# Performance work log

Measured on AMD Instinct MI355X. Metric: run time of the kernel, lower is better.

Reference implementation:

```python
import jax, jax.numpy as jnp
import numpy as np

DIM = 256; HEADS = 8; WS = 7; ALPHA = 0.5
HD = DIM // HEADS                      # head_dim = 32
GH = int(HEADS * ALPHA); LH = HEADS - GH   # 4 global / 4 local heads
GD = GH * HD; LD = LH * HD             # 128 / 128
HID = int(DIM * 4.0)                   # mlp hidden = 1024
SCALE = HD ** -0.5


def ln(x, g, b, eps=1e-5):
    m = jnp.mean(x, -1, keepdims=True)
    v = jnp.var(x, -1, keepdims=True)
    return (x - m) * jax.lax.rsqrt(v + eps) * g + b


def setup_inputs() -> dict:
    key = jax.random.key(0)
    ks = jax.random.split(key, 12)
    B, H, W = 4, 112, 112
    N = H * W
    def p(k, shape, s=0.02):
        return jax.random.normal(k, shape, jnp.float32) * s
    return {
        'x': jax.random.normal(ks[0], (B, N, DIM), jnp.float32),
        'x_reverse': jax.random.normal(ks[1], (B, N, DIM), jnp.float32),
        'g1': jnp.ones((DIM,), jnp.float32), 'b1': jnp.zeros((DIM,), jnp.float32),
        'g2': jnp.ones((DIM,), jnp.float32), 'b2': jnp.zeros((DIM,), jnp.float32),
        'Gq_w': p(ks[2], (DIM, GD)), 'Gq_b': jnp.zeros((GD,), jnp.float32),
        'Gkv_w': p(ks[3], (DIM, 2 * GD)), 'Gkv_b': jnp.zeros((2 * GD,), jnp.float32),
        'Gp_w': p(ks[4], (GD, GD)), 'Gp_b': jnp.zeros((GD,), jnp.float32),
        'Lq_w': p(ks[5], (DIM, LD)), 'Lq_b': jnp.zeros((LD,), jnp.float32),
        'Lkv_w': p(ks[6], (DIM, 2 * LD)), 'Lkv_b': jnp.zeros((2 * LD,), jnp.float32),
        'Lp_w': p(ks[7], (LD, LD)), 'Lp_b': jnp.zeros((LD,), jnp.float32),
        'fc1_w': p(ks[8], (DIM, HID)), 'fc1_b': jnp.zeros((HID,), jnp.float32),
        'dw_w': p(ks[9], (HID, 1, 3, 3), 0.05), 'dw_b': jnp.zeros((HID,), jnp.float32),
        'fc2_w': p(ks[10], (HID, DIM)), 'fc2_b': jnp.zeros((DIM,), jnp.float32),
        'H': 112, 'W': 112,
    }


def reference(x, x_reverse, g1, b1, g2, b2,
              Gq_w, Gq_b, Gkv_w, Gkv_b, Gp_w, Gp_b,
              Lq_w, Lq_b, Lkv_w, Lkv_b, Lp_w, Lp_b,
              fc1_w, fc1_b, dw_w, dw_b, fc2_w, fc2_b, H, W):
    B, N, C = x.shape
    assert H % WS == 0 and W % WS == 0  # shapes chosen so no padding branch
    xn = ln(x, g1, b1).reshape(B, H, W, C)
    xrn = ln(x_reverse, g1, b1).reshape(B, H, W, C)

    # ---- Global attention: queries from every pixel, kv from avg-pooled (ws x ws) grid
    q = (xn.reshape(B, N, C) @ Gq_w + Gq_b).reshape(B, N, GH, HD)
    pooled = xrn.reshape(B, H // WS, WS, W // WS, WS, C).mean(axis=(2, 4)).reshape(B, -1, C)
    kv = (pooled @ Gkv_w + Gkv_b).reshape(B, -1, 2, GH, HD)
    k, v = kv[:, :, 0], kv[:, :, 1]
    a = jax.nn.softmax(jnp.einsum('bnhd,bmhd->bhnm', q, k) * SCALE, axis=-1)
    g_out = jnp.einsum('bhnm,bmhd->bnhd', a, v).reshape(B, H, W, GD) @ Gp_w + Gp_b

    # ---- Local windowed attention (ws x ws non-overlapping windows)
    hg, wg = H // WS, W // WS
    TG, T = hg * wg, WS * WS
    def windows(t):
        return t.reshape(B, hg, WS, wg, WS, C).transpose(0, 1, 3, 2, 4, 5).reshape(B, TG, T, C)
    xw, xrw = windows(xn), windows(xrn)
    ql = (xw @ Lq_w + Lq_b).reshape(B, TG, T, LH, HD)
    kvl = (xrw @ Lkv_w + Lkv_b).reshape(B, TG, T, 2, LH, HD)
    kl, vl = kvl[:, :, :, 0], kvl[:, :, :, 1]
    al = jax.nn.softmax(jnp.einsum('bgqhd,bgkhd->bghqk', ql, kl) * SCALE, axis=-1)
    lo = jnp.einsum('bghqk,bgkhd->bgqhd', al, vl).reshape(B, hg, wg, WS, WS, LD)
    lo = lo.transpose(0, 1, 3, 2, 4, 5).reshape(B, H, W, LD) @ Lp_w + Lp_b

    x = x + jnp.concatenate([g_out, lo], axis=-1).reshape(B, N, C)

    # ---- DWMlp: fc1 -> depthwise 3x3 conv -> GELU -> fc2
    h = ln(x, g2, b2) @ fc1_w + fc1_b
    himg = h.reshape(B, H, W, HID).transpose(0, 3, 1, 2)
    himg = jax.lax.conv_general_dilated(
        himg, dw_w, (1, 1), 'SAME', feature_group_count=HID,
        dimension_numbers=('NCHW', 'OIHW', 'NCHW')) + dw_b[None, :, None, None]
    h = jax.nn.gelu(himg.reshape(B, HID, N).transpose(0, 2, 1), approximate=False)
    return x + (h @ fc2_w + fc2_b)
```

## Files before the change

### kernel.cpp

```cpp
#include <hip/hip_runtime.h>
#include <hip/hip_bf16.h>
#include <math.h>

typedef __hip_bfloat16 bf16;
typedef __attribute__((ext_vector_type(8))) short bf16x8;
typedef __attribute__((ext_vector_type(4))) float f32x4;

static constexpr int B_  = 4;
static constexpr int Hh  = 112, Ww = 112;
static constexpr int Nn  = Hh * Ww;
static constexpr int Cc  = 256;
static constexpr int M_  = B_ * Nn;
static constexpr int GH_ = 4;
static constexpr int GD_ = 128;
static constexpr int LD_ = 128;
static constexpr int HID_ = 1024;
static constexpr int TG_ = 256;
static constexpr int T__ = 49;
static constexpr float SCALE_ = 0.17677669529663687f;

__device__ __forceinline__ float toF(const bf16 v)  { return __bfloat162float(v); }
__device__ __forceinline__ float toF(const float v) { return v; }
__device__ __forceinline__ void st_out(float* p, float v) { *p = v; }
__device__ __forceinline__ void st_out(bf16* p, float v)  { *p = __float2bfloat16(v); }

__device__ __forceinline__ void gload_lds16(const bf16* g, bf16* l) {
  using gvoid = const __attribute__((address_space(1))) void;
  using lvoid = __attribute__((address_space(3))) void;
  __builtin_amdgcn_global_load_lds((gvoid*)g, (lvoid*)l, 16, 0, 0);
}

__device__ __forceinline__ int win_row_map(int r) {
  int b  = r / Nn;
  int rr = r - b * Nn;
  int g  = rr / T__;
  int t  = rr - g * T__;
  int gh = g >> 4, gw = g & 15;
  int i  = t / 7,  j  = t - i * 7;
  int n  = (gh * 7 + i) * Ww + gw * 7 + j;
  return b * Nn + n;
}

__global__ void guard_fill_kernel(float* out) {
  out[threadIdx.x + blockIdx.x * 256] = 1.0e6f;
}

__global__ __launch_bounds__(256) void convert_all_kernel(
    const float* __restrict__ s0, const float* __restrict__ s1,
    const float* __restrict__ s2, const float* __restrict__ s3,
    const float* __restrict__ s4, const float* __restrict__ s5,
    const float* __restrict__ s6, const float* __restrict__ s7,
    bf16* __restrict__ wt) {
  int idx = blockIdx.x * 256 + threadIdx.x;
  const float* W; int K, N, base;
  if      (idx < 32768)  { W = s0; K = 256;  N = 128;  base = 0; }
  else if (idx < 98304)  { W = s1; K = 256;  N = 256;  base = 32768; }
  else if (idx < 114688) { W = s2; K = 128;  N = 128;  base = 98304; }
  else if (idx < 147456) { W = s3; K = 256;  N = 128;  base = 114688; }
  else if (idx < 212992) { W = s4; K = 256;  N = 256;  base = 147456; }
  else if (idx < 229376) { W = s5; K = 128;  N = 128;  base = 212992; }
  else if (idx < 491520) { W = s6; K = 256;  N = 1024; base = 229376; }
  else                   { W = s7; K = 1024; N = 256;  base = 491520; }
  int loc = idx - base;
  int n = loc / K, k = loc - n * K;
  wt[idx] = __float2bfloat16(W[(size_t)k * N + n]);
}

__global__ __launch_bounds__(256) void ln_dual_kernel(const float* __restrict__ x,
                                                      const float* __restrict__ xr,
                                                      const float* __restrict__ g,
                                                      const float* __restrict__ bta,
                                                      bf16* __restrict__ xn,
                                                      bf16* __restrict__ xrn) {
  const int tid = threadIdx.x;
  const int row = blockIdx.x * 4 + (tid >> 6);
  const int lane = tid & 63;
  const int c0 = lane * 4;
  const float* src = blockIdx.y ? xr : x;
  bf16* dst = blockIdx.y ? xrn : xn;
  float4 v = *(const float4*)(src + (size_t)row * Cc + c0);
  float s  = v.x + v.y + v.z + v.w;
  float ss = v.x * v.x + v.y * v.y + v.z * v.z + v.w * v.w;
  #pragma unroll
  for (int off = 1; off < 64; off <<= 1) {
    s  += __shfl_xor(s, off);
    ss += __shfl_xor(ss, off);
  }
  float mean = s * (1.0f / Cc);
  float var  = ss * (1.0f / Cc) - mean * mean;
  float r = rsqrtf(var + 1e-5f);
  float4 gv = *(const float4*)(g + c0);
  float4 bv = *(const float4*)(bta + c0);
  bf16 o[4];
  o[0] = __float2bfloat16((v.x - mean) * r * gv.x + bv.x);
  o[1] = __float2bfloat16((v.y - mean) * r * gv.y + bv.y);
  o[2] = __float2bfloat16((v.z - mean) * r * gv.z + bv.z);
  o[3] = __float2bfloat16((v.w - mean) * r * gv.w + bv.w);
  *(uint2*)(dst + (size_t)row * Cc + c0) = *(uint2*)o;
}

__global__ __launch_bounds__(64) void pool_kernel(const bf16* __restrict__ xrn,
                                                  bf16* __restrict__ pooled) {
  const int lane = threadIdx.x;
  const int c0 = lane * 4;
  const int g  = blockIdx.x;
  const int b  = blockIdx.y;
  const int gh = g >> 4, gw = g & 15;
  float acc[4] = {};
  union U4 { uint2 u; bf16 e[4]; };
  #pragma unroll
  for (int i = 0; i < 7; i++)
    for (int j = 0; j < 7; j++) {
      int n = (gh * 7 + i) * Ww + gw * 7 + j;
      U4 r4;
      r4.u = *(const uint2*)(xrn + ((size_t)b * Nn + n) * Cc + c0);
      #pragma unroll
      for (int u = 0; u < 4; u++) acc[u] += toF(r4.e[u]);
    }
  bf16 o[4];
  #pragma unroll
  for (int u = 0; u < 4; u++) o[u] = __float2bfloat16(acc[u] * (1.0f / 49.0f));
  *(uint2*)(pooled + ((size_t)b * TG_ + g) * Cc + c0) = *(uint2*)o;
}

template <typename OutT, bool WIN_A, bool RES>
__global__ __launch_bounds__(256) void mfma_gemm_kernel(const bf16* __restrict__ A,
                                                        const bf16* __restrict__ Wt,
                                                        const float* __restrict__ bias,
                                                        const float* __restrict__ res,
                                                        OutT* __restrict__ out,
                                                        int M, int N, int K) {
  __shared__ __align__(16) bf16 As[128 * 32];
  __shared__ __align__(16) bf16 Bs[128 * 32];
  const int tid = threadIdx.x;
  const int bm = blockIdx.y * 128, bn = blockIdx.x * 128;
  const int lane = tid & 63, w = tid >> 6;
  const int wm = (w >> 1) * 64, wn = (w & 1) * 64;

  const int srow0 = w * 32 + (lane >> 2);
  const int srow1 = srow0 + 16;
  const int kq    = (lane & 3) * 8;
  const int ar0 = bm + srow0, ar1 = bm + srow1;
  const int as0 = WIN_A ? win_row_map(ar0) : ar0;
  const int as1 = WIN_A ? win_row_map(ar1) : ar1;
  const bf16* Ag0 = A  + (size_t)as0 * K + kq;
  const bf16* Ag1 = A  + (size_t)as1 * K + kq;
  const bf16* Bg0 = Wt + (size_t)(bn + srow0) * K + kq;
  const bf16* Bg1 = Wt + (size_t)(bn + srow1) * K + kq;
  bf16* Al0 = &As[srow0 * 32 + kq];
  bf16* Al1 = &As[srow1 * 32 + kq];
  bf16* Bl0 = &Bs[srow0 * 32 + kq];
  bf16* Bl1 = &Bs[srow1 * 32 + kq];

  f32x4 acc[4][4];
  #pragma unroll
  for (int i = 0; i < 4; i++)
    #pragma unroll
    for (int j = 0; j < 4; j++) acc[i][j] = (f32x4){0.f, 0.f, 0.f, 0.f};

  const int r16  = lane & 15;
  const int koct = (lane >> 4) * 8;
  const int mrow = wm + r16;
  const int nrow = wn + r16;

  for (int k0 = 0; k0 < K; k0 += 32) {
    gload_lds16(Ag0 + k0, Al0);
    gload_lds16(Ag1 + k0, Al1);
    gload_lds16(Bg0 + k0, Bl0);
    gload_lds16(Bg1 + k0, Bl1);
    __syncthreads();
    bf16x8 af[4], bfr[4];
    #pragma unroll
    for (int i = 0; i < 4; i++) af[i]  = *(const bf16x8*)&As[(mrow + i * 16) * 32 + koct];
    #pragma unroll
    for (int j = 0; j < 4; j++) bfr[j] = *(const bf16x8*)&Bs[(nrow + j * 16) * 32 + koct];
    #pragma unroll
    for (int i = 0; i < 4; i++)
      #pragma unroll
      for (int j = 0; j < 4; j++)
        acc[i][j] = __builtin_amdgcn_mfma_f32_16x16x32_bf16(af[i], bfr[j], acc[i][j], 0, 0, 0);
    __syncthreads();
  }

  const int r0 = (lane >> 4) * 4;
  #pragma unroll
  for (int j = 0; j < 4; j++) {
    const int col = bn + wn + j * 16 + r16;
    const float bv = bias[col];
    #pragma unroll
    for (int i = 0; i < 4; i++) {
      const int rowb = bm + wm + i * 16 + r0;
      #pragma unroll
      for (int r = 0; r < 4; r++) {
        size_t ro = (size_t)(rowb + r) * N + col;
        float v = acc[i][j][r] + bv;
        if (RES) v += res[ro];
        st_out(out + ro, v);
      }
    }
  }
}

__global__ __launch_bounds__(256) void gattn_kernel(const bf16* __restrict__ q,
                                                    const bf16* __restrict__ kv,
                                                    bf16* __restrict__ out) {
  __shared__ __align__(16) bf16 Ks[256][40];
  __shared__ __align__(16) bf16 Vt[32][264];
  __shared__ __align__(16) bf16 Ps[4][32][40];
  const int tid = threadIdx.x;
  const int lane = tid & 63, w = tid >> 6;
  const int h = blockIdx.y, b = blockIdx.z;
  const int n0 = blockIdx.x * 128;
  const int r16 = lane & 15, oct = (lane >> 4) * 8;
  const bf16* kvb = kv + (size_t)b * TG_ * 256;

  {
    const int key = tid;
    const bf16* kp = kvb + (size_t)key * 256 + h * 32;
    *(uint4*)&Ks[key][0]  = *(const uint4*)(kp);
    *(uint4*)&Ks[key][8]  = *(const uint4*)(kp + 8);
    *(uint4*)&Ks[key][16] = *(const uint4*)(kp + 16);
    *(uint4*)&Ks[key][24] = *(const uint4*)(kp + 24);
    union { uint4 u[4]; bf16 e[32]; } vv;
    vv.u[0] = *(const uint4*)(kp + 128);
    vv.u[1] = *(const uint4*)(kp + 136);
    vv.u[2] = *(const uint4*)(kp + 144);
    vv.u[3] = *(const uint4*)(kp + 152);
    #pragma unroll
    for (int d = 0; d < 32; d++) Vt[d][key] = vv.e[d];
  }
  const size_t qbase0 = ((size_t)(b * Nn + n0 + w * 32 + r16)) * GD_ + h * 32 + oct;
  bf16x8 aq0 = *(const bf16x8*)(q + qbase0);
  bf16x8 aq1 = *(const bf16x8*)(q + qbase0 + (size_t)16 * GD_);
  __syncthreads();

  f32x4 rs0 = {0.f, 0.f, 0.f, 0.f}, rs1 = {0.f, 0.f, 0.f, 0.f};
  f32x4 ov[2][2];
  #pragma unroll
  for (int i = 0; i < 2; i++)
    #pragma unroll
    for (int dt = 0; dt < 2; dt++) ov[i][dt] = (f32x4){0.f, 0.f, 0.f, 0.f};

  for (int c0 = 0; c0 < 256; c0 += 32) {
    #pragma unroll
    for (int t = 0; t < 2; t++) {
      bf16x8 bk = *(const bf16x8*)&Ks[c0 + t * 16 + r16][oct];
      f32x4 s0 = __builtin_amdgcn_mfma_f32_16x16x32_bf16(aq0, bk, (f32x4){0.f,0.f,0.f,0.f}, 0, 0, 0);
      f32x4 s1 = __builtin_amdgcn_mfma_f32_16x16x32_bf16(aq1, bk, (f32x4){0.f,0.f,0.f,0.f}, 0, 0, 0);
      const int prow = (lane >> 4) * 4;
      const int pcol = t * 16 + r16;
      #pragma unroll
      for (int r = 0; r < 4; r++) {
        bf16 pb0 = __float2bfloat16(__expf(s0[r] * SCALE_));
        bf16 pb1 = __float2bfloat16(__expf(s1[r] * SCALE_));
        rs0[r] += toF(pb0);
        rs1[r] += toF(pb1);
        Ps[w][prow + r][pcol]      = pb0;
        Ps[w][16 + prow + r][pcol] = pb1;
      }
    }
    bf16x8 ap0 = *(const bf16x8*)&Ps[w][r16][oct];
    bf16x8 ap1 = *(const bf16x8*)&Ps[w][16 + r16][oct];
    #pragma unroll
    for (int dt = 0; dt < 2; dt++) {
      bf16x8 bv = *(const bf16x8*)&Vt[dt * 16 + r16][c0 + oct];
      ov[0][dt] = __builtin_amdgcn_mfma_f32_16x16x32_bf16(ap0, bv, ov[0][dt], 0, 0, 0);
      ov[1][dt] = __builtin_amdgcn_mfma_f32_16x16x32_bf16(ap1, bv, ov[1][dt], 0, 0, 0);
    }
  }
  #pragma unroll
  for (int off = 1; off < 16; off <<= 1) {
    #pragma unroll
    for (int r = 0; r < 4; r++) {
      rs0[r] += __shfl_xor(rs0[r], off);
      rs1[r] += __shfl_xor(rs1[r], off);
    }
  }
  const int orow0 = b * Nn + n0 + w * 32 + (lane >> 4) * 4;
  #pragma unroll
  for (int r = 0; r < 4; r++) {
    float inv0 = 1.0f / rs0[r];
    float inv1 = 1.0f / rs1[r];
    size_t ro0 = (size_t)(orow0 + r) * GD_ + h * 32;
    size_t ro1 = ro0 + (size_t)16 * GD_;
    #pragma unroll
    for (int dt = 0; dt < 2; dt++) {
      out[ro0 + dt * 16 + r16] = __float2bfloat16(ov[0][dt][r] * inv0);
      out[ro1 + dt * 16 + r16] = __float2bfloat16(ov[1][dt][r] * inv1);
    }
  }
}

__global__ __launch_bounds__(256) void lattn_kernel(const bf16* __restrict__ ql,
                                                    const bf16* __restrict__ kvl,
                                                    bf16* __restrict__ out) {
  __shared__ __align__(16) bf16 Ks[4][64][40];
  __shared__ __align__(16) bf16 Vt[4][32][72];
  __shared__ __align__(16) bf16 Ps[4][64][72];
  const int tid = threadIdx.x;
  const int lane = tid & 63, w = tid >> 6;
  const int g = blockIdx.x, b = blockIdx.y;
  const int r16 = lane & 15, oct = (lane >> 4) * 8;
  const size_t wbase = ((size_t)b * TG_ + g) * T__;

  for (int u = tid; u < T__ * 32; u += 256) {
    int m = u >> 5, c8 = u & 31;
    union { uint4 q4; bf16 e[8]; } ch;
    ch.q4 = *(const uint4*)(kvl + (wbase + m) * 256 + c8 * 8);
    if (c8 < 16) {
      int h = c8 >> 2, d0 = (c8 & 3) * 8;
      *(uint4*)&Ks[h][m][d0] = ch.q4;
    } else {
      int cv = c8 - 16;
      int h = cv >> 2, d0 = (cv & 3) * 8;
      #pragma unroll
      for (int e = 0; e < 8; e++) Vt[h][d0 + e][m] = ch.e[e];
    }
  }
  for (int z = tid; z < 4 * 32 * 15; z += 256) {
    int h = z / 480, rem = z - h * 480;
    int d = rem / 15, key = 49 + (rem - d * 15);
    Vt[h][d][key] = __float2bfloat16(0.f);
  }
  bf16x8 aq[4];
  #pragma unroll
  for (int i = 0; i < 4; i++) {
    int qr = 16 * i + r16;
    if (qr > 48) qr = 48;
    aq[i] = *(const bf16x8*)(ql + (wbase + qr) * LD_ + w * 32 + oct);
  }
  __syncthreads();

  f32x4 s[4][4];
  #pragma unroll
  for (int j = 0; j < 4; j++) {
    bf16x8 bk = *(const bf16x8*)&Ks[w][16 * j + r16][oct];
    #pragma unroll
    for (int i = 0; i < 4; i++)
      s[i][j] = __builtin_amdgcn_mfma_f32_16x16x32_bf16(aq[i], bk, (f32x4){0.f,0.f,0.f,0.f}, 0, 0, 0);
  }

  const int prow = (lane >> 4) * 4;
  float rs[4][4];
  #pragma unroll
  for (int i = 0; i < 4; i++) {
    #pragma unroll
    for (int r = 0; r < 4; r++) {
      float acc = 0.f;
      #pragma unroll
      for (int j = 0; j < 4; j++) {
        float p = __expf(s[i][j][r] * SCALE_);
        if (j == 3 && r16 != 0) p = 0.f;
        bf16 pb = __float2bfloat16(p);
        Ps[w][16 * i + prow + r][16 * j + r16] = pb;
        acc += toF(pb);
      }
      #pragma unroll
      for (int off = 1; off < 16; off <<= 1) acc += __shfl_xor(acc, off);
      rs[i][r] = acc;
    }
  }

  f32x4 ov[4][2];
  #pragma unroll
  for (int i = 0; i < 4; i++) {
    ov[i][0] = (f32x4){0.f, 0.f, 0.f, 0.f};
    ov[i][1] = (f32x4){0.f, 0.f, 0.f, 0.f};
  }
  #pragma unroll
  for (int kc = 0; kc < 2; kc++) {
    bf16x8 bv0 = *(const bf16x8*)&Vt[w][r16][kc * 32 + oct];
    bf16x8 bv1 = *(const bf16x8*)&Vt[w][16 + r16][kc * 32 + oct];
    #pragma unroll
    for (int i = 0; i < 4; i++) {
      bf16x8 ap = *(const bf16x8*)&Ps[w][16 * i + r16][kc * 32 + oct];
      ov[i][0] = __builtin_amdgcn_mfma_f32_16x16x32_bf16(ap, bv0, ov[i][0], 0, 0, 0);
      ov[i][1] = __builtin_amdgcn_mfma_f32_16x16x32_bf16(ap, bv1, ov[i][1], 0, 0, 0);
    }
  }

  #pragma unroll
  for (int i = 0; i < 4; i++) {
    #pragma unroll
    for (int r = 0; r < 4; r++) {
      int qr = 16 * i + prow + r;
      if (qr < T__) {
        float inv = 1.0f / rs[i][r];
        size_t o = (wbase + qr) * LD_ + w * 32;
        out[o + r16]      = __float2bfloat16(ov[i][0][r] * inv);
        out[o + 16 + r16] = __float2bfloat16(ov[i][1][r] * inv);
      }
    }
  }
}

__global__ __launch_bounds__(256) void combine_ln_kernel(const float* __restrict__ x,
                                                         const bf16* __restrict__ gout,
                                                         const bf16* __restrict__ lo_w,
                                                         const float* __restrict__ g2,
                                                         const float* __restrict__ b2,
                                                         float* __restrict__ xres,
                                                         bf16* __restrict__ xn2) {
  const int tid = threadIdx.x;
  const int row = blockIdx.x * 4 + (tid >> 6);
  const int lane = tid & 63;
  const int c0 = lane * 4;
  int b = row / Nn, n = row - b * Nn;
  int y = n / Ww, xx = n - y * Ww;
  int gh = y / 7, i = y - gh * 7;
  int gw = xx / 7, j = xx - gw * 7;
  size_t wrow = ((size_t)b * TG_ + gh * 16 + gw) * T__ + i * 7 + j;
  union U4 { uint2 u; bf16 e[4]; } r4;
  if (lane < 32) r4.u = *(const uint2*)(gout + (size_t)row * GD_ + c0);
  else           r4.u = *(const uint2*)(lo_w + wrow * LD_ + (c0 - 128));
  float4 v = *(const float4*)(x + (size_t)row * Cc + c0);
  v.x += toF(r4.e[0]); v.y += toF(r4.e[1]); v.z += toF(r4.e[2]); v.w += toF(r4.e[3]);
  *(float4*)(xres + (size_t)row * Cc + c0) = v;
  float s  = v.x + v.y + v.z + v.w;
  float ss = v.x * v.x + v.y * v.y + v.z * v.z + v.w * v.w;
  #pragma unroll
  for (int off = 1; off < 64; off <<= 1) {
    s  += __shfl_xor(s, off);
    ss += __shfl_xor(ss, off);
  }
  float mean = s * (1.0f / Cc);
  float var  = ss * (1.0f / Cc) - mean * mean;
  float r = rsqrtf(var + 1e-5f);
  float4 gv = *(const float4*)(g2 + c0);
  float4 bv = *(const float4*)(b2 + c0);
  bf16 o[4];
  o[0] = __float2bfloat16((v.x - mean) * r * gv.x + bv.x);
  o[1] = __float2bfloat16((v.y - mean) * r * gv.y + bv.y);
  o[2] = __float2bfloat16((v.z - mean) * r * gv.z + bv.z);
  o[3] = __float2bfloat16((v.w - mean) * r * gv.w + bv.w);
  *(uint2*)(xn2 + (size_t)row * Cc + c0) = *(uint2*)o;
}

static constexpr int TW_ = 14;
__global__ __launch_bounds__(256) void dwconv_gelu_kernel(const bf16* __restrict__ h1,
                                                          const float* __restrict__ w,
                                                          const float* __restrict__ bias,
                                                          bf16* __restrict__ h2) {
  const int tid = threadIdx.x;
  const int c0 = tid * 4;
  const int img = blockIdx.z, y = blockIdx.y;
  const int xt = blockIdx.x * TW_;
  const size_t ibase = (size_t)img * Nn * HID_;

  float wreg[9][4], breg[4];
  #pragma unroll
  for (int u = 0; u < 4; u++) {
    breg[u] = bias[c0 + u];
    #pragma unroll
    for (int t = 0; t < 9; t++) wreg[t][u] = w[(c0 + u) * 9 + t];
  }

  const bf16* rowp[3];
  bool rok[3];
  #pragma unroll
  for (int r = 0; r < 3; r++) {
    int yy = y - 1 + r;
    rok[r] = (yy >= 0 && yy < Hh);
    rowp[r] = h1 + ibase + (size_t)(rok[r] ? yy : 0) * Ww * HID_ + c0;
  }

  float wa[3][4], wb[3][4], wc[3][4];
  union U4 { ushort2 u2[2]; bf16 e[4]; };
  auto loadcol = [&](int xcol, float v[3][4]) {
    if (xcol < 0 || xcol >= Ww) {
      #pragma unroll
      for (int r = 0; r < 3; r++)
        #pragma unroll
        for (int u = 0; u < 4; u++) v[r][u] = 0.f;
      return;
    }
    #pragma unroll
    for (int r = 0; r < 3; r++) {
      if (rok[r]) {
        U4 raw;
        *(uint2*)&raw = *(const uint2*)(rowp[r] + (size_t)xcol * HID_);
        #pragma unroll
        for (int u = 0; u < 4; u++) v[r][u] = toF(raw.e[u]);
      } else {
        #pragma unroll
        for (int u = 0; u < 4; u++) v[r][u] = 0.f;
      }
    }
  };
  loadcol(xt - 1, wa);
  loadcol(xt, wb);

  for (int xx = 0; xx < TW_; xx++) {
    const int x = xt + xx;
    loadcol(x + 1, wc);
    bf16 res[4];
    #pragma unroll
    for (int u = 0; u < 4; u++) {
      float a = breg[u];
      a = fmaf(wa[0][u], wreg[0][u], a);
      a = fmaf(wb[0][u], wreg[1][u], a);
      a = fmaf(wc[0][u], wreg[2][u], a);
      a = fmaf(wa[1][u], wreg[3][u], a);
      a = fmaf(wb[1][u], wreg[4][u], a);
      a = fmaf(wc[1][u], wreg[5][u], a);
      a = fmaf(wa[2][u], wreg[6][u], a);
      a = fmaf(wb[2][u], wreg[7][u], a);
      a = fmaf(wc[2][u], wreg[8][u], a);
      float gl = 0.5f * a * (1.0f + erff(a * 0.7071067811865475f));
      res[u] = __float2bfloat16(gl);
    }
    *(uint2*)(h2 + ibase + (size_t)(y * Ww + x) * HID_ + c0) = *(uint2*)res;
    #pragma unroll
    for (int r = 0; r < 3; r++)
      #pragma unroll
      for (int u = 0; u < 4; u++) { wa[r][u] = wb[r][u]; wb[r][u] = wc[r][u]; }
  }
}

extern "C" void kernel_launch(void* const* d_in, const int* in_sizes, int n_in,
                              void* d_out, int out_size, void* d_ws, size_t ws_size,
                              hipStream_t stream) {
  const float* x     = (const float*)d_in[0];
  const float* xrev  = (const float*)d_in[1];
  const float* g1    = (const float*)d_in[2];
  const float* b1    = (const float*)d_in[3];
  const float* g2    = (const float*)d_in[4];
  const float* b2    = (const float*)d_in[5];
  const float* Gq_w  = (const float*)d_in[6];
  const float* Gq_b  = (const float*)d_in[7];
  const float* Gkv_w = (const float*)d_in[8];
  const float* Gkv_b = (const float*)d_in[9];
  const float* Gp_w  = (const float*)d_in[10];
  const float* Gp_b  = (const float*)d_in[11];
  const float* Lq_w  = (const float*)d_in[12];
  const float* Lq_b  = (const float*)d_in[13];
  const float* Lkv_w = (const float*)d_in[14];
  const float* Lkv_b = (const float*)d_in[15];
  const float* Lp_w  = (const float*)d_in[16];
  const float* Lp_b  = (const float*)d_in[17];
  const float* fc1_w = (const float*)d_in[18];
  const float* fc1_b = (const float*)d_in[19];
  const float* dw_w  = (const float*)d_in[20];
  const float* dw_b  = (const float*)d_in[21];
  const float* fc2_w = (const float*)d_in[22];
  const float* fc2_b = (const float*)d_in[23];

  const size_t E_GQ = 256 * 128, E_GKV = 256 * 256, E_GP = 128 * 128;
  const size_t E_LQ = 256 * 128, E_LKV = 256 * 256, E_LP = 128 * 128;
  const size_t E_F1 = 256 * 1024, E_F2 = 1024 * 256;
  char* ws = (char*)d_ws;
  bf16* Gq_t  = (bf16*)ws;
  bf16* Gkv_t = Gq_t  + E_GQ;
  bf16* Gp_t  = Gkv_t + E_GKV;
  bf16* Lq_t  = Gp_t  + E_GP;
  bf16* Lkv_t = Lq_t  + E_LQ;
  bf16* Lp_t  = Lkv_t + E_LKV;
  bf16* f1_t  = Lp_t  + E_LP;
  bf16* f2_t  = f1_t  + E_F1;
  const size_t WT_ELEMS = E_GQ + E_GKV + E_GP + E_LQ + E_LKV + E_LP + E_F1 + E_F2;
  const size_t WT_BYTES = WT_ELEMS * 2;

  const size_t SZ_ROW2 = (size_t)M_ * Cc * 2;
  const size_t SZ_HALF = (size_t)M_ * 128 * 2;
  const size_t SZ_POOL = (size_t)B_ * TG_ * Cc * 2;
  const size_t SZ_KVG  = (size_t)B_ * TG_ * 256 * 2;
  const size_t SZ_H    = (size_t)(2 * Nn) * HID_ * 2;
  char* arena = ws + WT_BYTES;
  bf16* S1 = (bf16*)(arena);
  bf16* S2 = (bf16*)(arena + SZ_ROW2);
  bf16* S3 = (bf16*)(arena + 2 * SZ_ROW2);
  bf16* S4 = (bf16*)(arena + 2 * SZ_ROW2 + SZ_HALF);
  bf16* S5 = (bf16*)(arena + 2 * SZ_ROW2 + 2 * SZ_HALF);
  bf16* poolb = (bf16*)(arena + 2 * SZ_ROW2 + 3 * SZ_HALF);
  bf16* kvG   = (bf16*)(arena + 2 * SZ_ROW2 + 3 * SZ_HALF + SZ_POOL);
  const size_t ARENA_A = 2 * SZ_ROW2 + 3 * SZ_HALF + SZ_POOL + SZ_KVG;
  bf16* xn2 = S1;
  bf16* h1  = (bf16*)(arena + SZ_ROW2);
  bf16* h2  = (bf16*)(arena + SZ_ROW2 + SZ_H);
  const size_t ARENA_B = SZ_ROW2 + 2 * SZ_H;

  float* out  = (float*)d_out;
  float* xres = (float*)d_out;
  const size_t NEED = WT_BYTES + (ARENA_A > ARENA_B ? ARENA_A : ARENA_B);
  if (ws_size < NEED) {
    guard_fill_kernel<<<16, 256, 0, stream>>>(out);
    return;
  }

  bf16* xn = S1;  bf16* xrn = S2;  bf16* qbuf = S3;  bf16* gattn = S4;  bf16* gout = S5;
  bf16* kvl = S1; bf16* lo_w = S2; bf16* qlb  = S3;  bf16* lattn = S4;

  convert_all_kernel<<<2944, 256, 0, stream>>>(Gq_w, Gkv_w, Gp_w, Lq_w, Lkv_w, Lp_w,
                                               fc1_w, fc2_w, (bf16*)ws);
  ln_dual_kernel<<<dim3(M_ / 4, 2), 256, 0, stream>>>(x, xrev, g1, b1, xn, xrn);
  pool_kernel<<<dim3(TG_, B_), 64, 0, stream>>>(xrn, poolb);
  mfma_gemm_kernel<bf16, false, false><<<dim3(1, M_ / 128), 256, 0, stream>>>(
      xn, Gq_t, Gq_b, nullptr, qbuf, M_, 128, 256);
  mfma_gemm_kernel<bf16, false, false><<<dim3(2, 8), 256, 0, stream>>>(
      poolb, Gkv_t, Gkv_b, nullptr, kvG, 1024, 256, 256);
  gattn_kernel<<<dim3(Nn / 128, GH_, B_), 256, 0, stream>>>(qbuf, kvG, gattn);
  mfma_gemm_kernel<bf16, false, false><<<dim3(1, M_ / 128), 256, 0, stream>>>(
      gattn, Gp_t, Gp_b, nullptr, gout, M_, 128, 128);
  mfma_gemm_kernel<bf16, true, false><<<dim3(1, M_ / 128), 256, 0, stream>>>(
      xn, Lq_t, Lq_b, nullptr, qlb, M_, 128, 256);
  mfma_gemm_kernel<bf16, true, false><<<dim3(2, M_ / 128), 256, 0, stream>>>(
      xrn, Lkv_t, Lkv_b, nullptr, kvl, M_, 256, 256);
  lattn_kernel<<<dim3(TG_, B_), 256, 0, stream>>>(qlb, kvl, lattn);
  mfma_gemm_kernel<bf16, false, false><<<dim3(1, M_ / 128), 256, 0, stream>>>(
      lattn, Lp_t, Lp_b, nullptr, lo_w, M_, 128, 128);
  combine_ln_kernel<<<M_ / 4, 256, 0, stream>>>(x, gout, lo_w, g2, b2, xres, xn2);
  for (int half = 0; half < 2; half++) {
    const size_t r0 = (size_t)half * 2 * Nn;
    mfma_gemm_kernel<bf16, false, false><<<dim3(8, (2 * Nn) / 128), 256, 0, stream>>>(
        xn2 + r0 * Cc, f1_t, fc1_b, nullptr, h1, 2 * Nn, 1024, 256);
    dwconv_gelu_kernel<<<dim3(Ww / TW_, Hh, 2), 256, 0, stream>>>(h1, dw_w, dw_b, h2);
    mfma_gemm_kernel<float, false, true><<<dim3(2, (2 * Nn) / 128), 256, 0, stream>>>(
        h2, f2_t, fc2_b, xres + r0 * Cc, out + r0 * Cc, 2 * Nn, 256, 1024);
  }
}
```

Baseline: 542.8 us.

## Retile depthwise conv to 1x2 output patches with all loads issued upfront

The depthwise 3x3 conv+GELU kernel no longer walks 14 columns with a sliding register window. Each block now computes two vertically adjacent outputs for one column, loading the 4x3 neighborhood at once. This raises the block count and exposes more independent loads to hide latency. In exchange, each input is fetched about twice as often, relying on cache to absorb the redundancy.

```diff
diff --git a/kernel.cpp b/kernel.cpp
--- a/kernel.cpp
+++ b/kernel.cpp
@@ -436,16 +436,15 @@
   *(uint2*)(xn2 + (size_t)row * Cc + c0) = *(uint2*)o;
 }
 
-static constexpr int TW_ = 14;
 __global__ __launch_bounds__(256) void dwconv_gelu_kernel(const bf16* __restrict__ h1,
                                                           const float* __restrict__ w,
                                                           const float* __restrict__ bias,
                                                           bf16* __restrict__ h2) {
   const int tid = threadIdx.x;
   const int c0 = tid * 4;
-  const int img = blockIdx.z, y = blockIdx.y;
-  const int xt = blockIdx.x * TW_;
-  const size_t ibase = (size_t)img * Nn * HID_;
+  const int x  = blockIdx.x;
+  const int y0 = blockIdx.y * 2;
+  const size_t ibase = (size_t)blockIdx.z * Nn * HID_;
 
   float wreg[9][4], breg[4];
   #pragma unroll
@@ -455,65 +454,41 @@
     for (int t = 0; t < 9; t++) wreg[t][u] = w[(c0 + u) * 9 + t];
   }
 
-  const bf16* rowp[3];
-  bool rok[3];
-  #pragma unroll
-  for (int r = 0; r < 3; r++) {
-    int yy = y - 1 + r;
-    rok[r] = (yy >= 0 && yy < Hh);
-    rowp[r] = h1 + ibase + (size_t)(rok[r] ? yy : 0) * Ww * HID_ + c0;
-  }
-
-  float wa[3][4], wb[3][4], wc[3][4];
-  union U4 { ushort2 u2[2]; bf16 e[4]; };
-  auto loadcol = [&](int xcol, float v[3][4]) {
-    if (xcol < 0 || xcol >= Ww) {
+  float v[4][3][4];
+  union U4 { uint2 u; bf16 e[4]; };
+  #pragma unroll
+  for (int r = 0; r < 4; r++) {
+    const int yy = y0 - 1 + r;
+    const bool rv = (yy >= 0) && (yy < Hh);
+    const int yc = rv ? yy : 0;
+    #pragma unroll
+    for (int c = 0; c < 3; c++) {
+      const int xx = x - 1 + c;
+      const bool cvld = (xx >= 0) && (xx < Ww);
+      const int xc = cvld ? xx : 0;
+      U4 raw;
+      raw.u = *(const uint2*)(h1 + ibase + ((size_t)yc * Ww + xc) * HID_ + c0);
+      if (!(rv && cvld)) { raw.u.x = 0u; raw.u.y = 0u; }
+      #pragma unroll
+      for (int u = 0; u < 4; u++) v[r][c][u] = toF(raw.e[u]);
+    }
+  }
+
+  #pragma unroll
+  for (int p = 0; p < 2; p++) {
+    bf16 res[4];
+    #pragma unroll
+    for (int u = 0; u < 4; u++) {
+      float a = breg[u];
       #pragma unroll
       for (int r = 0; r < 3; r++)
         #pragma unroll
-        for (int u = 0; u < 4; u++) v[r][u] = 0.f;
-      return;
-    }
-    #pragma unroll
-    for (int r = 0; r < 3; r++) {
-      if (rok[r]) {
-        U4 raw;
-        *(uint2*)&raw = *(const uint2*)(rowp[r] + (size_t)xcol * HID_);
-        #pragma unroll
-        for (int u = 0; u < 4; u++) v[r][u] = toF(raw.e[u]);
-      } else {
-        #pragma unroll
-        for (int u = 0; u < 4; u++) v[r][u] = 0.f;
-      }
-    }
-  };
-  loadcol(xt - 1, wa);
-  loadcol(xt, wb);
-
-  for (int xx = 0; xx < TW_; xx++) {
-    const int x = xt + xx;
-    loadcol(x + 1, wc);
-    bf16 res[4];
-    #pragma unroll
-    for (int u = 0; u < 4; u++) {
-      float a = breg[u];
-      a = fmaf(wa[0][u], wreg[0][u], a);
-      a = fmaf(wb[0][u], wreg[1][u], a);
-      a = fmaf(wc[0][u], wreg[2][u], a);
-      a = fmaf(wa[1][u], wreg[3][u], a);
-      a = fmaf(wb[1][u], wreg[4][u], a);
-      a = fmaf(wc[1][u], wreg[5][u], a);
-      a = fmaf(wa[2][u], wreg[6][u], a);
-      a = fmaf(wb[2][u], wreg[7][u], a);
-      a = fmaf(wc[2][u], wreg[8][u], a);
+        for (int c = 0; c < 3; c++)
+          a = fmaf(v[p + r][c][u], wreg[r * 3 + c][u], a);
       float gl = 0.5f * a * (1.0f + erff(a * 0.7071067811865475f));
       res[u] = __float2bfloat16(gl);
     }
-    *(uint2*)(h2 + ibase + (size_t)(y * Ww + x) * HID_ + c0) = *(uint2*)res;
-    #pragma unroll
-    for (int r = 0; r < 3; r++)
-      #pragma unroll
-      for (int u = 0; u < 4; u++) { wa[r][u] = wb[r][u]; wb[r][u] = wc[r][u]; }
+    *(uint2*)(h2 + ibase + ((size_t)(y0 + p) * Ww + x) * HID_ + c0) = *(uint2*)res;
   }
 }
 
@@ -613,7 +588,7 @@
     const size_t r0 = (size_t)half * 2 * Nn;
     mfma_gemm_kernel<bf16, false, false><<<dim3(8, (2 * Nn) / 128), 256, 0, stream>>>(
         xn2 + r0 * Cc, f1_t, fc1_b, nullptr, h1, 2 * Nn, 1024, 256);
-    dwconv_gelu_kernel<<<dim3(Ww / TW_, Hh, 2), 256, 0, stream>>>(h1, dw_w, dw_b, h2);
+    dwconv_gelu_kernel<<<dim3(Ww, Hh / 2, 2), 256, 0, stream>>>(h1, dw_w, dw_b, h2);
     mfma_gemm_kernel<float, false, true><<<dim3(2, (2 * Nn) / 128), 256, 0, stream>>>(
         h2, f2_t, fc2_b, xres + r0 * Cc, out + r0 * Cc, 2 * Nn, 256, 1024);
   }
```

New measurement: 595.5 us. 9.7% more time.
